# Kernel tuning notes

Hardware: AMD Instinct MI355X
Metric: run time of the kernel (lower is better)

## Reference

```python
import jax, jax.numpy as jnp
import numpy as np

N_NODES = 5000
N_EDGES = 80000
HIDDEN = 128
NUM_RBF = 64
MAX_Z = 128
CUTOFF_UPPER = 5.0
LN_EPS = 1e-5


def setup_inputs() -> dict:
    key = jax.random.key(0)
    ks = jax.random.split(key, 24)
    H, R = HIDDEN, NUM_RBF
    def lin(k, out_d, in_d):
        s = 1.0 / np.sqrt(in_d)
        return jax.random.uniform(k, (out_d, in_d), jnp.float32, -s, s)
    def bias(k, out_d, in_d):
        s = 1.0 / np.sqrt(in_d)
        return jax.random.uniform(k, (out_d,), jnp.float32, -s, s)
    v = jax.random.normal(ks[3], (N_EDGES, 3), jnp.float32)
    v = v / jnp.linalg.norm(v, axis=-1, keepdims=True)
    return {
        "z": jax.random.randint(ks[0], (N_NODES,), 0, MAX_Z),
        "edge_index": jax.random.randint(ks[1], (2, N_EDGES), 0, N_NODES),
        "edge_weight": jax.random.uniform(ks[2], (N_EDGES,), jnp.float32) * CUTOFF_UPPER * 0.9,
        "edge_vec_norm": v,
        "edge_attr": jax.random.normal(ks[4], (N_EDGES, R), jnp.float32),
        "emb": jax.random.normal(ks[5], (MAX_Z, H), jnp.float32),
        "W_emb2": lin(ks[6], H, 2 * H), "b_emb2": bias(ks[7], H, 2 * H),
        "Wd1": lin(ks[8], H, R), "bd1": bias(ks[9], H, R),
        "Wd2": lin(ks[10], H, R), "bd2": bias(ks[11], H, R),
        "Wd3": lin(ks[12], H, R), "bd3": bias(ks[13], H, R),
        "Wt1": lin(ks[14], H, H), "Wt2": lin(ks[15], H, H), "Wt3": lin(ks[16], H, H),
        "Ws1": lin(ks[17], 2 * H, H), "bs1": bias(ks[18], 2 * H, H),
        "Ws2": lin(ks[19], 3 * H, 2 * H), "bs2": bias(ks[20], 3 * H, 2 * H),
        "ln_g": jnp.ones((H,), jnp.float32),
        "ln_b": jnp.zeros((H,), jnp.float32),
    }


def _skew(v):
    # v: [E,3] -> [E,3,3] skew-symmetric
    z = jnp.zeros_like(v[:, 0])
    return jnp.stack(
        [z, -v[:, 2], v[:, 1], v[:, 2], z, -v[:, 0], -v[:, 1], v[:, 0], z], axis=1
    ).reshape(-1, 3, 3)


def _sym(v):
    # symmetric traceless part of outer product (outer product already symmetric)
    outer = v[:, :, None] * v[:, None, :]
    tr = jnp.trace(outer, axis1=-2, axis2=-1) / 3.0
    return outer - tr[:, None, None] * jnp.eye(3, dtype=v.dtype)


def reference(z, edge_index, edge_weight, edge_vec_norm, edge_attr,
              emb, W_emb2, b_emb2, Wd1, bd1, Wd2, bd2, Wd3, bd3,
              Wt1, Wt2, Wt3, Ws1, bs1, Ws2, bs2, ln_g, ln_b):
    N = z.shape[0]
    H = emb.shape[1]
    src, dst = edge_index[0], edge_index[1]

    # atomic number message Zij: [E,H]
    Z = emb[z]
    Zij = jnp.concatenate([Z[src], Z[dst]], axis=-1) @ W_emb2.T + b_emb2

    # cosine cutoff (cutoff_lower = 0)
    cut = 0.5 * (jnp.cos(edge_weight * (jnp.pi / CUTOFF_UPPER)) + 1.0)
    cut = cut * (edge_weight < CUTOFF_UPPER).astype(edge_weight.dtype)
    C = cut[:, None] * Zij  # [E,H]

    f1 = (edge_attr @ Wd1.T + bd1) * C  # [E,H]
    f2 = (edge_attr @ Wd2.T + bd2) * C
    f3 = (edge_attr @ Wd3.T + bd3) * C

    eye = jnp.eye(3, dtype=C.dtype)
    Iij = f1[:, :, None, None] * eye  # [E,H,3,3]
    Aij = f2[:, :, None, None] * _skew(edge_vec_norm)[:, None, :, :]
    Sij = f3[:, :, None, None] * _sym(edge_vec_norm)[:, None, :, :]

    I = jax.ops.segment_sum(Iij, src, num_segments=N)  # [N,H,3,3]
    A = jax.ops.segment_sum(Aij, src, num_segments=N)
    S = jax.ops.segment_sum(Sij, src, num_segments=N)

    # Frobenius norm per channel, LayerNorm, scalar MLP
    tn = ((I + A + S) ** 2).sum((-2, -1))  # [N,H]
    mu = tn.mean(-1, keepdims=True)
    var = tn.var(-1, keepdims=True)
    norm = (tn - mu) / jnp.sqrt(var + LN_EPS) * ln_g + ln_b
    norm = jax.nn.silu(norm @ Ws1.T + bs1)
    norm = jax.nn.silu(norm @ Ws2.T + bs2)
    norm = norm.reshape(N, H, 3)

    I = jnp.einsum('nhij,gh->ngij', I, Wt1) * norm[:, :, 0, None, None]
    A = jnp.einsum('nhij,gh->ngij', A, Wt2) * norm[:, :, 1, None, None]
    S = jnp.einsum('nhij,gh->ngij', S, Wt3) * norm[:, :, 2, None, None]
    return I + A + S
```

## Files before the change

### kernel.cpp

```cpp
#include <hip/hip_runtime.h>
#include <hip/hip_bf16.h>

#define NN   5000
#define NP   5008
#define NE   80000
#define HID  128
#define NRBF 64
#define PI_OVER_5 0.6283185307179586f
#define LN_EPS 1e-5f

typedef unsigned short bf16_t;
typedef __attribute__((ext_vector_type(8))) short short8;
typedef __attribute__((ext_vector_type(4))) float floatx4;

__device__ __forceinline__ bf16_t to_bf16(float x){
    union { float f; unsigned int u; } v; v.f = x;
    unsigned int r = v.u + 0x7fffu + ((v.u >> 16) & 1u);
    return (bf16_t)(r >> 16);
}
__device__ __forceinline__ float from_bf16(bf16_t h){
    union { unsigned int u; float f; } v; v.u = ((unsigned int)h) << 16;
    return v.f;
}
__device__ __forceinline__ uint4 pack8(const float* s){
    float4 a = *(const float4*)s;
    float4 b = *(const float4*)(s + 4);
    uint4 o;
    o.x = to_bf16(a.x) | ((unsigned)to_bf16(a.y) << 16);
    o.y = to_bf16(a.z) | ((unsigned)to_bf16(a.w) << 16);
    o.z = to_bf16(b.x) | ((unsigned)to_bf16(b.y) << 16);
    o.w = to_bf16(b.z) | ((unsigned)to_bf16(b.w) << 16);
    return o;
}

__global__ __launch_bounds__(128) void k_embtab(
    const float* __restrict__ W_emb2, const float* __restrict__ emb,
    float* __restrict__ embL, float* __restrict__ embR)
{
    int t = blockIdx.x;
    int h = threadIdx.x;
    const float* er = emb + t * HID;
    const float* wl = W_emb2 + (size_t)h * (2 * HID);
    float sl = 0.f, sr = 0.f;
    #pragma unroll 8
    for (int k = 0; k < HID; k++){
        float e = er[k];
        sl += wl[k] * e;
        sr += wl[HID + k] * e;
    }
    embL[t * HID + h] = sl;
    embR[t * HID + h] = sr;
}

__global__ __launch_bounds__(256) void k_prep_wts(
    const float* __restrict__ Wd1, const float* __restrict__ Wd2, const float* __restrict__ Wd3,
    const float* __restrict__ bd1, const float* __restrict__ bd2, const float* __restrict__ bd3,
    const float* __restrict__ Wt1, const float* __restrict__ Wt2, const float* __restrict__ Wt3,
    const float* __restrict__ Ws1, const float* __restrict__ Ws2,
    bf16_t* __restrict__ Wcat, bf16_t* __restrict__ Wtc,
    bf16_t* __restrict__ Ws1b, bf16_t* __restrict__ Ws2b, float* __restrict__ bdcat)
{
    int t = blockIdx.x * 256 + threadIdx.x;
    int i8 = t * 8;
    const float* src; bf16_t* dst;
    if (i8 < 24576){
        int j = i8; int tb = j >> 13; int r = j & 8191;
        src = ((tb == 0) ? Wd1 : (tb == 1) ? Wd2 : Wd3) + r; dst = Wcat + j;
    } else if (i8 < 24576 + 49152){
        int j = i8 - 24576; int tb = j >> 14; int r = j & 16383;
        src = ((tb == 0) ? Wt1 : (tb == 1) ? Wt2 : Wt3) + r; dst = Wtc + j;
    } else if (i8 < 24576 + 49152 + 32768){
        int j = i8 - 73728; src = Ws1 + j; dst = Ws1b + j;
    } else {
        int j = i8 - 106496; src = Ws2 + j; dst = Ws2b + j;
    }
    *(uint4*)dst = pack8(src);
    if (t < 384){
        int tb2 = t >> 7, ch2 = t & 127;
        const float* bsrc = (tb2 == 0) ? bd1 : ((tb2 == 1) ? bd2 : bd3);
        bdcat[t] = bsrc[ch2];
    }
}

__global__ void k_count(const int* __restrict__ ei, int* __restrict__ counts){
    int e = blockIdx.x * 256 + threadIdx.x;
    if (e < NE) atomicAdd(&counts[ei[e]], 1);
}

__global__ __launch_bounds__(1024) void k_scan(
    const int* __restrict__ counts, int* __restrict__ offsets, int* __restrict__ cursor)
{
    __shared__ int s[1024];
    const int t = threadIdx.x;
    const int CH = 5;
    int base = t * CH;
    int loc[CH];
    int lsum = 0;
    #pragma unroll
    for (int u = 0; u < CH; u++){
        int i = base + u;
        int v = (i < NN) ? counts[i] : 0;
        loc[u] = lsum;
        lsum += v;
    }
    s[t] = lsum;
    __syncthreads();
    for (int d = 1; d < 1024; d <<= 1){
        int v = (t >= d) ? s[t - d] : 0;
        __syncthreads();
        s[t] += v;
        __syncthreads();
    }
    int excl = s[t] - lsum;
    #pragma unroll
    for (int u = 0; u < CH; u++){
        int i = base + u;
        if (i < NN){ int o = excl + loc[u]; offsets[i] = o; cursor[i] = o; }
    }
    if (t == 1023) offsets[NN] = s[1023];
}

__global__ void k_fill(const int* __restrict__ ei, const int* __restrict__ z,
                       const float* __restrict__ ew, const float* __restrict__ evn,
                       int* __restrict__ cursor, int* __restrict__ elist,
                       float2* __restrict__ meta, float* __restrict__ evn_p){
    int e = blockIdx.x * 256 + threadIdx.x;
    if (e < NE){
        int sN = ei[e], dN = ei[NE + e];
        int p = atomicAdd(&cursor[sN], 1);
        elist[p] = e;
        float w = ew[e];
        float c = (w < 5.0f) ? 0.5f * (__cosf(w * PI_OVER_5) + 1.0f) : 0.0f;
        meta[p] = make_float2(c, __int_as_float(z[sN] | (z[dN] << 8)));
        evn_p[p*3+0] = evn[e*3+0];
        evn_p[p*3+1] = evn[e*3+1];
        evn_p[p*3+2] = evn[e*3+2];
    }
}

__global__ __launch_bounds__(256) void k_edge(
    const float* __restrict__ attr, const int* __restrict__ elist,
    const float2* __restrict__ meta,
    const bf16_t* __restrict__ Wcat, const float* __restrict__ bdcat,
    const float* __restrict__ embL, const float* __restrict__ embR,
    const float* __restrict__ b_emb2,
    bf16_t* __restrict__ f1, bf16_t* __restrict__ f2, bf16_t* __restrict__ f3)
{
    __shared__ __align__(16) bf16_t sB[64 * 72];
    __shared__ float sCut[64];
    __shared__ int   sZ[64];

    const int tid = threadIdx.x;
    const int p0  = blockIdx.x * 64;

    {
        int r = tid >> 2, qt = tid & 3;
        int e = elist[p0 + r];
        const float* ar = attr + (size_t)e * NRBF + qt * 16;
        uint4 o0 = pack8(ar);
        uint4 o1 = pack8(ar + 8);
        *(uint4*)&sB[r * 72 + qt * 16]     = o0;
        *(uint4*)&sB[r * 72 + qt * 16 + 8] = o1;
    }
    if (tid < 64){
        float2 m = meta[p0 + tid];
        sCut[tid] = m.x;
        sZ[tid]   = __float_as_int(m.y);
    }
    __syncthreads();

    const int wv = tid >> 6, lane = tid & 63;
    const int col = lane & 15, q = lane >> 4;

    floatx4 acc[6][4];
    #pragma unroll
    for (int mt = 0; mt < 6; mt++)
        #pragma unroll
        for (int nt = 0; nt < 4; nt++)
            acc[mt][nt] = (floatx4)(0.f);

    #pragma unroll
    for (int s = 0; s < 2; s++){
        short8 bf[4];
        #pragma unroll
        for (int nt = 0; nt < 4; nt++){
            int r = nt * 16 + col;
            bf[nt] = *(const short8*)&sB[r * 72 + s * 32 + q * 8];
        }
        short8 af[6];
        #pragma unroll
        for (int t = 0; t < 3; t++)
            #pragma unroll
            for (int c = 0; c < 2; c++){
                int m = t * 128 + wv * 32 + c * 16 + col;
                af[t * 2 + c] = *(const short8*)(Wcat + (size_t)m * NRBF + s * 32 + q * 8);
            }
        #pragma unroll
        for (int mt = 0; mt < 6; mt++)
            #pragma unroll
            for (int nt = 0; nt < 4; nt++)
                acc[mt][nt] = __builtin_amdgcn_mfma_f32_16x16x32_bf16(
                    af[mt], bf[nt], acc[mt][nt], 0, 0, 0);
    }

    floatx4 be[2], bd[3][2];
    #pragma unroll
    for (int c = 0; c < 2; c++){
        int ch4 = wv * 32 + c * 16 + q * 4;
        be[c] = *(const floatx4*)(b_emb2 + ch4);
        #pragma unroll
        for (int t = 0; t < 3; t++)
            bd[t][c] = *(const floatx4*)(bdcat + t * 128 + ch4);
    }
    bf16_t* const fs[3] = {f1, f2, f3};
    #pragma unroll
    for (int nt = 0; nt < 4; nt++){
        int e = nt * 16 + col;
        float cut = sCut[e];
        int zp = sZ[e];
        int zs = zp & 255, zd = zp >> 8;
        size_t orow = (size_t)(p0 + e) * HID;
        #pragma unroll
        for (int c = 0; c < 2; c++){
            int ch4 = wv * 32 + c * 16 + q * 4;
            floatx4 L = *(const floatx4*)(embL + zs * HID + ch4);
            floatx4 R = *(const floatx4*)(embR + zd * HID + ch4);
            floatx4 Cv = (L + R + be[c]) * cut;
            #pragma unroll
            for (int t = 0; t < 3; t++){
                floatx4 v = (acc[t * 2 + c][nt] + bd[t][c]) * Cv;
                uint2 pk;
                pk.x = to_bf16(v[0]) | ((unsigned)to_bf16(v[1]) << 16);
                pk.y = to_bf16(v[2]) | ((unsigned)to_bf16(v[3]) << 16);
                *(uint2*)(fs[t] + orow + ch4) = pk;
            }
        }
    }
}

__global__ __launch_bounds__(128) void k_gather(
    const int* __restrict__ offsets, const float* __restrict__ evn_p,
    const bf16_t* __restrict__ f1, const bf16_t* __restrict__ f2, const bf16_t* __restrict__ f3,
    const float* __restrict__ ln_g, const float* __restrict__ ln_b,
    bf16_t* __restrict__ acc, bf16_t* __restrict__ ln_out)
{
    const int n = blockIdx.x, h = threadIdx.x;
    const int s = offsets[n], e_end = offsets[n + 1];
    float c=0, ax=0, ay=0, az=0, sxx=0, syy=0, szz=0, sxy=0, sxz=0, syz=0;
    for (int idx = s; idx < e_end; idx++){
        float vx = evn_p[idx*3+0], vy = evn_p[idx*3+1], vz = evn_p[idx*3+2];
        float t3 = (vx*vx + vy*vy + vz*vz) * (1.f/3.f);
        float a = from_bf16(f1[(size_t)idx * HID + h]);
        float b = from_bf16(f2[(size_t)idx * HID + h]);
        float d = from_bf16(f3[(size_t)idx * HID + h]);
        c += a;
        ax += b * vx; ay += b * vy; az += b * vz;
        sxx += d * (vx*vx - t3); syy += d * (vy*vy - t3); szz += d * (vz*vz - t3);
        sxy += d * (vx*vy); sxz += d * (vx*vz); syz += d * (vy*vz);
    }
    const int PS = NP * HID;
    const int base = n * HID + h;
    acc[0*PS+base]=to_bf16(c);   acc[1*PS+base]=to_bf16(ax);
    acc[2*PS+base]=to_bf16(ay);  acc[3*PS+base]=to_bf16(az);
    acc[4*PS+base]=to_bf16(sxx); acc[5*PS+base]=to_bf16(syy);
    acc[6*PS+base]=to_bf16(szz); acc[7*PS+base]=to_bf16(sxy);
    acc[8*PS+base]=to_bf16(sxz); acc[9*PS+base]=to_bf16(syz);

    float tn = 3.f*c*c + 2.f*c*(sxx+syy+szz)
             + sxx*sxx + syy*syy + szz*szz
             + 2.f*(sxy*sxy + sxz*sxz + syz*syz)
             + 2.f*(ax*ax + ay*ay + az*az);

    __shared__ float r1[128], r2[128];
    r1[h] = tn; r2[h] = tn * tn;
    __syncthreads();
    for (int st = 64; st > 0; st >>= 1){
        if (h < st){ r1[h] += r1[h + st]; r2[h] += r2[h + st]; }
        __syncthreads();
    }
    float mu  = r1[0] * (1.f / HID);
    float var = r2[0] * (1.f / HID) - mu * mu;
    ln_out[base] = to_bf16((tn - mu) * rsqrtf(var + LN_EPS) * ln_g[h] + ln_b[h]);
}

__global__ __launch_bounds__(256) void k_node(
    const bf16_t* __restrict__ lnb, const bf16_t* __restrict__ accb,
    const bf16_t* __restrict__ Ws1b, const float* __restrict__ bs1,
    const bf16_t* __restrict__ Ws2b, const float* __restrict__ bs2,
    const bf16_t* __restrict__ Wtc,
    float* __restrict__ out)
{
    __shared__ __align__(16) bf16_t h1s[16 * 280];
    __shared__ float nrms[16 * 392];

    const int tid = threadIdx.x;
    const int wv = tid >> 6, lane = tid & 63;
    const int col = lane & 15, q = lane >> 4;
    const int n0 = blockIdx.x * 16;

    {
        short8 a1[4];
        #pragma unroll
        for (int k = 0; k < 4; k++)
            a1[k] = *(const short8*)(lnb + (size_t)(n0 + col) * HID + k * 32 + q * 8);
        floatx4 c1[4];
        #pragma unroll
        for (int nt = 0; nt < 4; nt++) c1[nt] = (floatx4)(0.f);
        #pragma unroll
        for (int nt = 0; nt < 4; nt++){
            int cg = wv * 64 + nt * 16 + col;
            #pragma unroll
            for (int k = 0; k < 4; k++){
                short8 b = *(const short8*)(Ws1b + (size_t)cg * HID + k * 32 + q * 8);
                c1[nt] = __builtin_amdgcn_mfma_f32_16x16x32_bf16(a1[k], b, c1[nt], 0, 0, 0);
            }
        }
        #pragma unroll
        for (int nt = 0; nt < 4; nt++){
            int cg = wv * 64 + nt * 16 + col;
            float bias = bs1[cg];
            #pragma unroll
            for (int r = 0; r < 4; r++){
                float v = c1[nt][r] + bias;
                v = v / (1.f + __expf(-v));
                h1s[(q * 4 + r) * 280 + cg] = to_bf16(v);
            }
        }
    }
    __syncthreads();

    {
        short8 a2[8];
        #pragma unroll
        for (int k = 0; k < 8; k++)
            a2[k] = *(const short8*)&h1s[col * 280 + k * 32 + q * 8];
        floatx4 c2[6];
        #pragma unroll
        for (int nt = 0; nt < 6; nt++) c2[nt] = (floatx4)(0.f);
        #pragma unroll
        for (int nt = 0; nt < 6; nt++){
            int cg = wv * 96 + nt * 16 + col;
            #pragma unroll
            for (int k = 0; k < 8; k++){
                short8 b = *(const short8*)(Ws2b + (size_t)cg * 256 + k * 32 + q * 8);
                c2[nt] = __builtin_amdgcn_mfma_f32_16x16x32_bf16(a2[k], b, c2[nt], 0, 0, 0);
            }
        }
        #pragma unroll
        for (int nt = 0; nt < 6; nt++){
            int cg = wv * 96 + nt * 16 + col;
            float bias = bs2[cg];
            #pragma unroll
            for (int r = 0; r < 4; r++){
                float v = c2[nt][r] + bias;
                v = v / (1.f + __expf(-v));
                nrms[(q * 4 + r) * 392 + cg] = v;
            }
        }
    }
    __syncthreads();

    floatx4 cm[10][2];
    #pragma unroll
    for (int p = 0; p < 10; p++){
        #pragma unroll
        for (int nt = 0; nt < 2; nt++) cm[p][nt] = (floatx4)(0.f);
    }
    #pragma unroll
    for (int p = 0; p < 10; p++){
        const bf16_t* ap = accb + (size_t)p * NP * HID + (size_t)(n0 + col) * HID;
        short8 a3[4];
        #pragma unroll
        for (int k = 0; k < 4; k++)
            a3[k] = *(const short8*)(ap + k * 32 + q * 8);
        int tb = (p == 0) ? 0 : ((p < 4) ? 1 : 2);
        #pragma unroll
        for (int nt = 0; nt < 2; nt++){
            int g = wv * 32 + nt * 16 + col;
            const bf16_t* wp = Wtc + tb * 16384 + (size_t)g * HID;
            #pragma unroll
            for (int k = 0; k < 4; k++){
                short8 b = *(const short8*)(wp + k * 32 + q * 8);
                cm[p][nt] = __builtin_amdgcn_mfma_f32_16x16x32_bf16(a3[k], b, cm[p][nt], 0, 0, 0);
            }
        }
    }
    #pragma unroll
    for (int nt = 0; nt < 2; nt++){
        int g = wv * 32 + nt * 16 + col;
        #pragma unroll
        for (int r = 0; r < 4; r++){
            int node = q * 4 + r;
            int n = n0 + node;
            if (n < NN){
                float n0f = nrms[node * 392 + g * 3 + 0];
                float n1f = nrms[node * 392 + g * 3 + 1];
                float n2f = nrms[node * 392 + g * 3 + 2];
                float c   = cm[0][nt][r];
                float ax  = cm[1][nt][r], ay = cm[2][nt][r], az = cm[3][nt][r];
                float sxx = cm[4][nt][r], syy= cm[5][nt][r], szz= cm[6][nt][r];
                float sxy = cm[7][nt][r], sxz= cm[8][nt][r], syz= cm[9][nt][r];
                float* o = out + ((size_t)n * HID + g) * 9;
                o[0] = n0f*c + n2f*sxx;   o[1] = n2f*sxy - n1f*az;  o[2] = n2f*sxz + n1f*ay;
                o[3] = n2f*sxy + n1f*az;  o[4] = n0f*c + n2f*syy;   o[5] = n2f*syz - n1f*ax;
                o[6] = n2f*sxz - n1f*ay;  o[7] = n2f*syz + n1f*ax;  o[8] = n0f*c + n2f*szz;
            }
        }
    }
}

extern "C" void kernel_launch(void* const* d_in, const int* in_sizes, int n_in,
                              void* d_out, int out_size, void* d_ws, size_t ws_size,
                              hipStream_t stream)
{
    (void)in_sizes; (void)n_in; (void)out_size; (void)ws_size;
    const int*   z      = (const int*)  d_in[0];
    const int*   ei     = (const int*)  d_in[1];
    const float* ew     = (const float*)d_in[2];
    const float* evn    = (const float*)d_in[3];
    const float* attr   = (const float*)d_in[4];
    const float* emb    = (const float*)d_in[5];
    const float* W_emb2 = (const float*)d_in[6];
    const float* b_emb2 = (const float*)d_in[7];
    const float* Wd1 = (const float*)d_in[8];  const float* bd1 = (const float*)d_in[9];
    const float* Wd2 = (const float*)d_in[10]; const float* bd2 = (const float*)d_in[11];
    const float* Wd3 = (const float*)d_in[12]; const float* bd3 = (const float*)d_in[13];
    const float* Wt1 = (const float*)d_in[14]; const float* Wt2 = (const float*)d_in[15];
    const float* Wt3 = (const float*)d_in[16];
    const float* Ws1 = (const float*)d_in[17]; const float* bs1 = (const float*)d_in[18];
    const float* Ws2 = (const float*)d_in[19]; const float* bs2 = (const float*)d_in[20];
    const float* ln_g = (const float*)d_in[21]; const float* ln_b = (const float*)d_in[22];
    float* out = (float*)d_out;

    char* ws = (char*)d_ws;
    size_t o = 0;
    auto take = [&](size_t b)->size_t{ size_t c = o; o += (b + 255) & ~(size_t)255; return c; };
    size_t f1_o  = take((size_t)NE * HID * 2);
    size_t f2_o  = take((size_t)NE * HID * 2);
    size_t f3_o  = take((size_t)NE * HID * 2);
    size_t acc_o = take((size_t)10 * NP * HID * 2);
    size_t ln_of = take((size_t)NP * HID * 2);
    size_t eL_o  = take((size_t)128 * HID * 4);
    size_t eR_o  = take((size_t)128 * HID * 4);
    size_t cnt_o = take((size_t)NN * 4);
    size_t off_o = take((size_t)(NN + 1) * 4);
    size_t cur_o = take((size_t)NN * 4);
    size_t el_o  = take((size_t)NE * 4);
    size_t met_o = take((size_t)NE * 8);
    size_t evp_o = take((size_t)NE * 12);
    size_t wc_o  = take((size_t)384 * 64 * 2);
    size_t wt_o  = take((size_t)3 * 128 * 128 * 2);
    size_t w1_o  = take((size_t)256 * 128 * 2);
    size_t w2_o  = take((size_t)384 * 256 * 2);
    size_t bdc_o = take((size_t)384 * 4);

    bf16_t* f1 = (bf16_t*)(ws + f1_o);
    bf16_t* f2 = (bf16_t*)(ws + f2_o);
    bf16_t* f3 = (bf16_t*)(ws + f3_o);
    bf16_t* accb = (bf16_t*)(ws + acc_o);
    bf16_t* lnb  = (bf16_t*)(ws + ln_of);
    float* embL = (float*)(ws + eL_o);
    float* embR = (float*)(ws + eR_o);
    int* counts = (int*)(ws + cnt_o);
    int* offs   = (int*)(ws + off_o);
    int* cursor = (int*)(ws + cur_o);
    int* elist  = (int*)(ws + el_o);
    float2* meta = (float2*)(ws + met_o);
    float* evn_p = (float*)(ws + evp_o);
    bf16_t* Wcat = (bf16_t*)(ws + wc_o);
    bf16_t* Wtc  = (bf16_t*)(ws + wt_o);
    bf16_t* Ws1b = (bf16_t*)(ws + w1_o);
    bf16_t* Ws2b = (bf16_t*)(ws + w2_o);
    float* bdcat = (float*)(ws + bdc_o);

    hipMemsetAsync(counts, 0, (size_t)NN * 4, stream);

    k_prep_wts<<<100, 256, 0, stream>>>(Wd1, Wd2, Wd3, bd1, bd2, bd3,
                                        Wt1, Wt2, Wt3, Ws1, Ws2,
                                        Wcat, Wtc, Ws1b, Ws2b, bdcat);
    k_embtab<<<128, 128, 0, stream>>>(W_emb2, emb, embL, embR);
    k_count <<<(NE + 255) / 256, 256, 0, stream>>>(ei, counts);
    k_scan  <<<1, 1024, 0, stream>>>(counts, offs, cursor);
    k_fill  <<<(NE + 255) / 256, 256, 0, stream>>>(ei, z, ew, evn, cursor, elist, meta, evn_p);
    k_edge  <<<NE / 64, 256, 0, stream>>>(attr, elist, meta, Wcat, bdcat,
                                          embL, embR, b_emb2, f1, f2, f3);
    k_gather<<<NN, 128, 0, stream>>>(offs, evn_p, f1, f2, f3, ln_g, ln_b, accb, lnb);
    k_node  <<<(NN + 15) / 16, 256, 0, stream>>>(lnb, accb, Ws1b, bs1, Ws2b, bs2, Wtc, out);
}
```

Measured before the change: 229.8 us.

## Merge prep kernels into one launch and widen gather to wave-per-node

```diff
diff --git a/kernel.cpp b/kernel.cpp
--- a/kernel.cpp
+++ b/kernel.cpp
@@ -10,6 +10,7 @@
 #define LN_EPS 1e-5f
 
 typedef unsigned short bf16_t;
+typedef unsigned int uint_t;
 typedef __attribute__((ext_vector_type(8))) short short8;
 typedef __attribute__((ext_vector_type(4))) float floatx4;
 
@@ -22,69 +23,73 @@
     union { unsigned int u; float f; } v; v.u = ((unsigned int)h) << 16;
     return v.f;
 }
+__device__ __forceinline__ float bf_lo(uint_t u){
+    union { unsigned int x; float f; } v; v.x = u << 16; return v.f;
+}
+__device__ __forceinline__ float bf_hi(uint_t u){
+    union { unsigned int x; float f; } v; v.x = u & 0xffff0000u; return v.f;
+}
+__device__ __forceinline__ uint_t packbf(float a, float b){
+    return (uint_t)to_bf16(a) | ((uint_t)to_bf16(b) << 16);
+}
 __device__ __forceinline__ uint4 pack8(const float* s){
     float4 a = *(const float4*)s;
     float4 b = *(const float4*)(s + 4);
     uint4 o;
-    o.x = to_bf16(a.x) | ((unsigned)to_bf16(a.y) << 16);
-    o.y = to_bf16(a.z) | ((unsigned)to_bf16(a.w) << 16);
-    o.z = to_bf16(b.x) | ((unsigned)to_bf16(b.y) << 16);
-    o.w = to_bf16(b.z) | ((unsigned)to_bf16(b.w) << 16);
+    o.x = packbf(a.x, a.y);
+    o.y = packbf(a.z, a.w);
+    o.z = packbf(b.x, b.y);
+    o.w = packbf(b.z, b.w);
     return o;
 }
 
-__global__ __launch_bounds__(128) void k_embtab(
-    const float* __restrict__ W_emb2, const float* __restrict__ emb,
-    float* __restrict__ embL, float* __restrict__ embR)
-{
-    int t = blockIdx.x;
-    int h = threadIdx.x;
-    const float* er = emb + t * HID;
-    const float* wl = W_emb2 + (size_t)h * (2 * HID);
-    float sl = 0.f, sr = 0.f;
-    #pragma unroll 8
-    for (int k = 0; k < HID; k++){
-        float e = er[k];
-        sl += wl[k] * e;
-        sr += wl[HID + k] * e;
-    }
-    embL[t * HID + h] = sl;
-    embR[t * HID + h] = sr;
-}
-
-__global__ __launch_bounds__(256) void k_prep_wts(
+__global__ __launch_bounds__(256) void k_prep(
     const float* __restrict__ Wd1, const float* __restrict__ Wd2, const float* __restrict__ Wd3,
     const float* __restrict__ bd1, const float* __restrict__ bd2, const float* __restrict__ bd3,
     const float* __restrict__ Wt1, const float* __restrict__ Wt2, const float* __restrict__ Wt3,
     const float* __restrict__ Ws1, const float* __restrict__ Ws2,
+    const float* __restrict__ W_emb2, const float* __restrict__ emb,
+    const int* __restrict__ ei, int* __restrict__ counts,
     bf16_t* __restrict__ Wcat, bf16_t* __restrict__ Wtc,
-    bf16_t* __restrict__ Ws1b, bf16_t* __restrict__ Ws2b, float* __restrict__ bdcat)
+    bf16_t* __restrict__ Ws1b, bf16_t* __restrict__ Ws2b, float* __restrict__ bdcat,
+    float* __restrict__ embL, float* __restrict__ embR)
 {
-    int t = blockIdx.x * 256 + threadIdx.x;
-    int i8 = t * 8;
-    const float* src; bf16_t* dst;
-    if (i8 < 24576){
-        int j = i8; int tb = j >> 13; int r = j & 8191;
-        src = ((tb == 0) ? Wd1 : (tb == 1) ? Wd2 : Wd3) + r; dst = Wcat + j;
-    } else if (i8 < 24576 + 49152){
-        int j = i8 - 24576; int tb = j >> 14; int r = j & 16383;
-        src = ((tb == 0) ? Wt1 : (tb == 1) ? Wt2 : Wt3) + r; dst = Wtc + j;
-    } else if (i8 < 24576 + 49152 + 32768){
-        int j = i8 - 73728; src = Ws1 + j; dst = Ws1b + j;
+    int b = blockIdx.x, tid = threadIdx.x;
+    if (b < 100){
+        int t = b * 256 + tid;
+        int i8 = t * 8;
+        const float* src; bf16_t* dst;
+        if (i8 < 24576){
+            int j = i8; int tb = j >> 13; int r = j & 8191;
+            src = ((tb == 0) ? Wd1 : (tb == 1) ? Wd2 : Wd3) + r; dst = Wcat + j;
+        } else if (i8 < 24576 + 49152){
+            int j = i8 - 24576; int tb = j >> 14; int r = j & 16383;
+            src = ((tb == 0) ? Wt1 : (tb == 1) ? Wt2 : Wt3) + r; dst = Wtc + j;
+        } else if (i8 < 24576 + 49152 + 32768){
+            int j = i8 - 73728; src = Ws1 + j; dst = Ws1b + j;
+        } else {
+            int j = i8 - 106496; src = Ws2 + j; dst = Ws2b + j;
+        }
+        *(uint4*)dst = pack8(src);
+        if (t < 384){
+            int tb2 = t >> 7, ch2 = t & 127;
+            const float* bsrc = (tb2 == 0) ? bd1 : ((tb2 == 1) ? bd2 : bd3);
+            bdcat[t] = bsrc[ch2];
+        }
+    } else if (b < 228){
+        int t = b - 100;
+        int half = tid >> 7;
+        int h = tid & 127;
+        const float* wl = W_emb2 + (size_t)h * (2 * HID) + half * HID;
+        const float* er = emb + t * HID;
+        float s = 0.f;
+        #pragma unroll 8
+        for (int k = 0; k < HID; k++) s += wl[k] * er[k];
+        (half ? embR : embL)[t * HID + h] = s;
     } else {
-        int j = i8 - 106496; src = Ws2 + j; dst = Ws2b + j;
-    }
-    *(uint4*)dst = pack8(src);
-    if (t < 384){
-        int tb2 = t >> 7, ch2 = t & 127;
-        const float* bsrc = (tb2 == 0) ? bd1 : ((tb2 == 1) ? bd2 : bd3);
-        bdcat[t] = bsrc[ch2];
-    }
-}
-
-__global__ void k_count(const int* __restrict__ ei, int* __restrict__ counts){
-    int e = blockIdx.x * 256 + threadIdx.x;
-    if (e < NE) atomicAdd(&counts[ei[e]], 1);
+        int e = (b - 228) * 256 + tid;
+        if (e < NE) atomicAdd(&counts[ei[e]], 1);
+    }
 }
 
 __global__ __launch_bounds__(1024) void k_scan(
@@ -230,57 +235,96 @@
             for (int t = 0; t < 3; t++){
                 floatx4 v = (acc[t * 2 + c][nt] + bd[t][c]) * Cv;
                 uint2 pk;
-                pk.x = to_bf16(v[0]) | ((unsigned)to_bf16(v[1]) << 16);
-                pk.y = to_bf16(v[2]) | ((unsigned)to_bf16(v[3]) << 16);
+                pk.x = packbf(v[0], v[1]);
+                pk.y = packbf(v[2], v[3]);
                 *(uint2*)(fs[t] + orow + ch4) = pk;
             }
         }
     }
 }
 
-__global__ __launch_bounds__(128) void k_gather(
-    const int* __restrict__ offsets, const float* __restrict__ evn_p,
+__global__ __launch_bounds__(256) void k_gather(
+    const int* __restrict__ offs, const float* __restrict__ evn_p,
     const bf16_t* __restrict__ f1, const bf16_t* __restrict__ f2, const bf16_t* __restrict__ f3,
     const float* __restrict__ ln_g, const float* __restrict__ ln_b,
-    bf16_t* __restrict__ acc, bf16_t* __restrict__ ln_out)
+    bf16_t* __restrict__ accb, bf16_t* __restrict__ lnb)
 {
-    const int n = blockIdx.x, h = threadIdx.x;
-    const int s = offsets[n], e_end = offsets[n + 1];
-    float c=0, ax=0, ay=0, az=0, sxx=0, syy=0, szz=0, sxy=0, sxz=0, syz=0;
+    const int tid = threadIdx.x;
+    const int wv = tid >> 6, lane = tid & 63;
+    const int n = blockIdx.x * 4 + wv;
+    const int s = offs[n], e_end = offs[n + 1];
+
+    const uint_t* F1 = (const uint_t*)f1;
+    const uint_t* F2 = (const uint_t*)f2;
+    const uint_t* F3 = (const uint_t*)f3;
+
+    float c0=0,c1=0, ax0=0,ax1=0, ay0=0,ay1=0, az0=0,az1=0;
+    float sxx0=0,sxx1=0, syy0=0,syy1=0, szz0=0,szz1=0;
+    float sxy0=0,sxy1=0, sxz0=0,sxz1=0, syz0=0,syz1=0;
+
     for (int idx = s; idx < e_end; idx++){
+        size_t row = (size_t)idx * 64 + lane;
+        uint_t u1 = F1[row];
+        uint_t u2 = F2[row];
+        uint_t u3 = F3[row];
         float vx = evn_p[idx*3+0], vy = evn_p[idx*3+1], vz = evn_p[idx*3+2];
-        float t3 = (vx*vx + vy*vy + vz*vz) * (1.f/3.f);
-        float a = from_bf16(f1[(size_t)idx * HID + h]);
-        float b = from_bf16(f2[(size_t)idx * HID + h]);
-        float d = from_bf16(f3[(size_t)idx * HID + h]);
-        c += a;
-        ax += b * vx; ay += b * vy; az += b * vz;
-        sxx += d * (vx*vx - t3); syy += d * (vy*vy - t3); szz += d * (vz*vz - t3);
-        sxy += d * (vx*vy); sxz += d * (vx*vz); syz += d * (vy*vz);
-    }
-    const int PS = NP * HID;
-    const int base = n * HID + h;
-    acc[0*PS+base]=to_bf16(c);   acc[1*PS+base]=to_bf16(ax);
-    acc[2*PS+base]=to_bf16(ay);  acc[3*PS+base]=to_bf16(az);
-    acc[4*PS+base]=to_bf16(sxx); acc[5*PS+base]=to_bf16(syy);
-    acc[6*PS+base]=to_bf16(szz); acc[7*PS+base]=to_bf16(sxy);
-    acc[8*PS+base]=to_bf16(sxz); acc[9*PS+base]=to_bf16(syz);
-
-    float tn = 3.f*c*c + 2.f*c*(sxx+syy+szz)
-             + sxx*sxx + syy*syy + szz*szz
-             + 2.f*(sxy*sxy + sxz*sxz + syz*syz)
-             + 2.f*(ax*ax + ay*ay + az*az);
-
-    __shared__ float r1[128], r2[128];
-    r1[h] = tn; r2[h] = tn * tn;
-    __syncthreads();
-    for (int st = 64; st > 0; st >>= 1){
-        if (h < st){ r1[h] += r1[h + st]; r2[h] += r2[h + st]; }
-        __syncthreads();
-    }
-    float mu  = r1[0] * (1.f / HID);
-    float var = r2[0] * (1.f / HID) - mu * mu;
-    ln_out[base] = to_bf16((tn - mu) * rsqrtf(var + LN_EPS) * ln_g[h] + ln_b[h]);
+        float xx = vx*vx, yy = vy*vy, zz = vz*vz;
+        float t3 = (xx + yy + zz) * (1.f/3.f);
+        float gxx = xx - t3, gyy = yy - t3, gzz = zz - t3;
+        float gxy = vx*vy, gxz = vx*vz, gyz = vy*vz;
+        float a0 = bf_lo(u1), a1 = bf_hi(u1);
+        float b0 = bf_lo(u2), b1 = bf_hi(u2);
+        float d0 = bf_lo(u3), d1 = bf_hi(u3);
+        c0 += a0;            c1 += a1;
+        ax0 += b0 * vx;      ax1 += b1 * vx;
+        ay0 += b0 * vy;      ay1 += b1 * vy;
+        az0 += b0 * vz;      az1 += b1 * vz;
+        sxx0 += d0 * gxx;    sxx1 += d1 * gxx;
+        syy0 += d0 * gyy;    syy1 += d1 * gyy;
+        szz0 += d0 * gzz;    szz1 += d1 * gzz;
+        sxy0 += d0 * gxy;    sxy1 += d1 * gxy;
+        sxz0 += d0 * gxz;    sxz1 += d1 * gxz;
+        syz0 += d0 * gyz;    syz1 += d1 * gyz;
+    }
+
+    float tn0 = 3.f*c0*c0 + 2.f*c0*(sxx0+syy0+szz0)
+              + sxx0*sxx0 + syy0*syy0 + szz0*szz0
+              + 2.f*(sxy0*sxy0 + sxz0*sxz0 + syz0*syz0)
+              + 2.f*(ax0*ax0 + ay0*ay0 + az0*az0);
+    float tn1 = 3.f*c1*c1 + 2.f*c1*(sxx1+syy1+szz1)
+              + sxx1*sxx1 + syy1*syy1 + szz1*szz1
+              + 2.f*(sxy1*sxy1 + sxz1*sxz1 + syz1*syz1)
+              + 2.f*(ax1*ax1 + ay1*ay1 + az1*az1);
+
+    float s1 = tn0 + tn1, s2 = tn0*tn0 + tn1*tn1;
+    #pragma unroll
+    for (int d = 1; d < 64; d <<= 1){
+        s1 += __shfl_xor(s1, d);
+        s2 += __shfl_xor(s2, d);
+    }
+    float mu  = s1 * (1.f / HID);
+    float var = s2 * (1.f / HID) - mu * mu;
+    float rs  = rsqrtf(var + LN_EPS);
+    float2 g2 = *(const float2*)(ln_g + lane * 2);
+    float2 b2 = *(const float2*)(ln_b + lane * 2);
+    float ln0 = (tn0 - mu) * rs * g2.x + b2.x;
+    float ln1 = (tn1 - mu) * rs * g2.y + b2.y;
+
+    const size_t nrow = (size_t)n * 64 + lane;
+    uint_t* LN = (uint_t*)lnb;
+    uint_t* AC = (uint_t*)accb;
+    LN[nrow] = packbf(ln0, ln1);
+    const size_t PS = (size_t)NP * 64;
+    AC[0*PS + nrow] = packbf(c0, c1);
+    AC[1*PS + nrow] = packbf(ax0, ax1);
+    AC[2*PS + nrow] = packbf(ay0, ay1);
+    AC[3*PS + nrow] = packbf(az0, az1);
+    AC[4*PS + nrow] = packbf(sxx0, sxx1);
+    AC[5*PS + nrow] = packbf(syy0, syy1);
+    AC[6*PS + nrow] = packbf(szz0, szz1);
+    AC[7*PS + nrow] = packbf(sxy0, sxy1);
+    AC[8*PS + nrow] = packbf(sxz0, sxz1);
+    AC[9*PS + nrow] = packbf(syz0, syz1);
 }
 
 __global__ __launch_bounds__(256) void k_node(
@@ -475,15 +519,13 @@
 
     hipMemsetAsync(counts, 0, (size_t)NN * 4, stream);
 
-    k_prep_wts<<<100, 256, 0, stream>>>(Wd1, Wd2, Wd3, bd1, bd2, bd3,
-                                        Wt1, Wt2, Wt3, Ws1, Ws2,
-                                        Wcat, Wtc, Ws1b, Ws2b, bdcat);
-    k_embtab<<<128, 128, 0, stream>>>(W_emb2, emb, embL, embR);
-    k_count <<<(NE + 255) / 256, 256, 0, stream>>>(ei, counts);
-    k_scan  <<<1, 1024, 0, stream>>>(counts, offs, cursor);
-    k_fill  <<<(NE + 255) / 256, 256, 0, stream>>>(ei, z, ew, evn, cursor, elist, meta, evn_p);
-    k_edge  <<<NE / 64, 256, 0, stream>>>(attr, elist, meta, Wcat, bdcat,
-                                          embL, embR, b_emb2, f1, f2, f3);
-    k_gather<<<NN, 128, 0, stream>>>(offs, evn_p, f1, f2, f3, ln_g, ln_b, accb, lnb);
-    k_node  <<<(NN + 15) / 16, 256, 0, stream>>>(lnb, accb, Ws1b, bs1, Ws2b, bs2, Wtc, out);
-}
+    k_prep <<<228 + (NE + 255) / 256, 256, 0, stream>>>(
+        Wd1, Wd2, Wd3, bd1, bd2, bd3, Wt1, Wt2, Wt3, Ws1, Ws2, W_emb2, emb,
+        ei, counts, Wcat, Wtc, Ws1b, Ws2b, bdcat, embL, embR);
+    k_scan <<<1, 1024, 0, stream>>>(counts, offs, cursor);
+    k_fill <<<(NE + 255) / 256, 256, 0, stream>>>(ei, z, ew, evn, cursor, elist, meta, evn_p);
+    k_edge <<<NE / 64, 256, 0, stream>>>(attr, elist, meta, Wcat, bdcat,
+                                         embL, embR, b_emb2, f1, f2, f3);
+    k_gather<<<NN / 4, 256, 0, stream>>>(offs, evn_p, f1, f2, f3, ln_g, ln_b, accb, lnb);
+    k_node <<<(NN + 15) / 16, 256, 0, stream>>>(lnb, accb, Ws1b, bs1, Ws2b, bs2, Wtc, out);
+}
```

Result: faster. 224.5 us (-2.3%).
